# Performance work log

Measured on AMD Instinct MI355X. Metric: run time of the kernel, lower is better.

Reference implementation:

```python
import jax, jax.numpy as jnp
import numpy as np

N = 50000          # nodes
E = 1600000        # edges (avg degree 32)
H = 64             # hidden dim (module default x=64)
C = 10             # num_classes = max(y)+1
SLOPE = 0.01       # torch leaky_relu default


def _glorot(key, shape):
    lim = jnp.sqrt(6.0 / (shape[0] + shape[1]))
    return jax.random.uniform(key, shape, jnp.float32, -lim, lim)


def setup_inputs() -> dict:
    key = jax.random.key(0)
    ks = jax.random.split(key, 8)
    x = jax.random.normal(ks[0], (N, 1), jnp.float32)
    edge_index = jax.random.randint(ks[1], (2, E), 0, N, dtype=jnp.int64)
    W1 = _glorot(ks[2], (1, 10));  b1 = jnp.zeros((10,), jnp.float32)
    W2 = _glorot(ks[3], (10, H));  b2 = jnp.zeros((H,), jnp.float32)
    W3 = _glorot(ks[4], (H, H));   b3 = jnp.zeros((H,), jnp.float32)
    fcW = _glorot(ks[5], (H * N, C))
    fcb = jnp.zeros((C,), jnp.float32)
    return {"x": x, "edge_index": edge_index, "W1": W1, "b1": b1,
            "W2": W2, "b2": b2, "W3": W3, "b3": b3, "fcW": fcW, "fcb": fcb}


def _gcn_layer(h, W, b, src, dst, norm):
    # GCNConv: out = D^{-1/2} (A + I) D^{-1/2} (h W) + b
    h = h @ W                                   # [N, out]
    msg = h[src] * norm[:, None]                # gather + edge-scale
    agg = jax.ops.segment_sum(msg, dst, num_segments=N)  # scatter-add
    return agg + b


def reference(x, edge_index, W1, b1, W2, b2, W3, b3, fcW, fcb):
    src, dst = edge_index[0], edge_index[1]
    loop = jnp.arange(N, dtype=src.dtype)
    src_all = jnp.concatenate([src, loop])      # add self-loops
    dst_all = jnp.concatenate([dst, loop])
    deg = jax.ops.segment_sum(jnp.ones_like(dst_all, jnp.float32), dst_all,
                              num_segments=N)   # >= 1 due to self-loops
    dinv = jax.lax.rsqrt(deg)
    norm = dinv[src_all] * dinv[dst_all]        # per-edge normalization

    h = jax.nn.leaky_relu(_gcn_layer(x, W1, b1, src_all, dst_all, norm), SLOPE)
    h = jax.nn.leaky_relu(_gcn_layer(h, W2, b2, src_all, dst_all, norm), SLOPE)
    h = jax.nn.leaky_relu(_gcn_layer(h, W3, b3, src_all, dst_all, norm), SLOPE)

    logits = h.reshape(-1) @ fcW + fcb          # [C]
    return jax.nn.softmax(logits, axis=0)
```

## Files before the change

### kernel.cpp

```cpp
#include <hip/hip_runtime.h>
#include <hip/hip_fp16.h>
#include <hip/hip_fp8.h>


constexpr int F1  = 10;
constexpr int F1P = 16;
constexpr int HD  = 64;
constexpr int NC  = 10;
constexpr int LOGIT_BLOCKS = 2048;

constexpr int BSH   = 7;
constexpr int NBC   = 391;
constexpr int BCAPG = 5120;
constexpr int CSTR  = 16;
constexpr int LCAP  = 38;
constexpr int TILE  = 8192;

static __device__ __forceinline__ float lrelu(float v) {
    return v > 0.0f ? v : 0.01f * v;
}

#if defined(__has_builtin)
#if __has_builtin(__builtin_amdgcn_cvt_f32_fp8)
#define FP8_DECODE(w, c) __builtin_amdgcn_cvt_f32_fp8((int)(w), (c))
#endif
#endif
#ifndef FP8_DECODE
static __device__ __forceinline__ float fp8_decode_sw(unsigned w, int c) {
    __hip_fp8_e4m3 t; t.__x = (unsigned char)(w >> (8 * c)); return (float)t;
}
#define FP8_DECODE(w, c) fp8_decode_sw((w), (c))
#endif

static __device__ __forceinline__ unsigned char fp8_encode(float v) {
    __hip_fp8_e4m3 t(v);
    return (unsigned char)t.__x;
}

__global__ void k_bcur(int* __restrict__ bcur, int NB) {
    int b = blockIdx.x * blockDim.x + threadIdx.x;
    if (b < NB) bcur[b * CSTR] = b * BCAPG;
}

__global__ __launch_bounds__(512) void k_bucket(const int* __restrict__ src,
                                                const int* __restrict__ dst,
                                                int* __restrict__ bcur,
                                                unsigned* __restrict__ bpairs, int E) {
    __shared__ unsigned stage[NBC * LCAP];
    __shared__ int lcnt[NBC];
    for (int i = threadIdx.x; i < NBC; i += 512) lcnt[i] = 0;
    __syncthreads();
    int tile0 = blockIdx.x * TILE;
#pragma unroll
    for (int k = 0; k < TILE / 512; ++k) {
        int e = tile0 + k * 512 + threadIdx.x;
        if (e < E) {
            int d = dst[e];
            unsigned pk = (unsigned)src[e] | ((unsigned)(d & 127) << 16);
            int bb = d >> BSH;
            int pos = atomicAdd(&lcnt[bb], 1);
            if (pos < LCAP) stage[bb * LCAP + pos] = pk;
            else {
                int gp = atomicAdd(&bcur[bb * CSTR], 1);
                bpairs[gp] = pk;
            }
        }
    }
    __syncthreads();
    int wid = threadIdx.x >> 6, lane = threadIdx.x & 63;
    for (int bb = wid; bb < NBC; bb += 8) {
        int cntb = min(lcnt[bb], LCAP);
        if (cntb == 0) continue;
        int gp = 0;
        if (lane == 0) gp = atomicAdd(&bcur[bb * CSTR], cntb);
        gp = __shfl(gp, 0, 64);
        for (int i = lane; i < cntb; i += 64) bpairs[gp + i] = stage[bb * LCAP + i];
    }
}

__global__ __launch_bounds__(256) void k_fine(const int* __restrict__ bcur,
                                              const unsigned* __restrict__ bpairs,
                                              const float* __restrict__ x,
                                              unsigned short* __restrict__ csr,
                                              float* __restrict__ dinv,
                                              float* __restrict__ xs,
                                              int* __restrict__ rowbeg,
                                              int* __restrict__ rowend, int N) {
    __shared__ unsigned short lout[BCAPG];
    __shared__ int lcnt[128], lbeg[128];
    int b = blockIdx.x;
    int n0 = b << BSH;
    int nn = min(128, N - n0);
    int base = b * BCAPG;
    int nedges = bcur[b * CSTR] - base;
    for (int i = threadIdx.x; i < nn; i += 256) lcnt[i] = 0;
    __syncthreads();
    for (int i = threadIdx.x; i < nedges; i += 256)
        atomicAdd(&lcnt[(bpairs[base + i] >> 16) & 127], 1);
    __syncthreads();
    if (threadIdx.x == 0) {
        int acc = 0;
        for (int j = 0; j < nn; ++j) { lbeg[j] = acc; acc += lcnt[j]; }
    }
    __syncthreads();
    for (int i = threadIdx.x; i < nn; i += 256) {
        int node = n0 + i;
        float di = rsqrtf(1.0f + (float)lcnt[i]);
        dinv[node]   = di;
        xs[node]     = x[node] * di;
        rowbeg[node] = base + lbeg[i];
        rowend[node] = base + lbeg[i] + lcnt[i];
    }
    __syncthreads();
    for (int i = threadIdx.x; i < nn; i += 256) lcnt[i] = lbeg[i];
    __syncthreads();
    for (int i = threadIdx.x; i < nedges; i += 256) {
        unsigned p = bpairs[base + i];
        int pos = atomicAdd(&lcnt[(p >> 16) & 127], 1);
        lout[pos] = (unsigned short)(p & 0xFFFFu);
    }
    __syncthreads();
    for (int i = threadIdx.x; i < nedges; i += 256) csr[base + i] = lout[i];
}

__global__ void k_l1h1(const int* __restrict__ rowbeg, const int* __restrict__ rowend,
                       const unsigned short* __restrict__ csr,
                       const float* __restrict__ xs, const float* __restrict__ dinv,
                       const float* __restrict__ W1, const float* __restrict__ b1,
                       __half* __restrict__ h1s, int N) {
    int node = (blockIdx.x * blockDim.x + threadIdx.x) >> 6;
    int lane = threadIdx.x & 63;
    if (node >= N) return;
    int lo = rowbeg[node], hi = rowend[node];
    float acc = 0.0f;
    for (int j = lo + lane; j < hi; j += 64) acc += xs[csr[j]];
#pragma unroll
    for (int off = 32; off > 0; off >>= 1) acc += __shfl_xor(acc, off, 64);
    float di = dinv[node];
    float s = di * (acc + xs[node]);
    if (lane < F1P) {
        float h = (lane < F1) ? lrelu(s * W1[lane] + b1[lane]) * di : 0.0f;
        h1s[node * F1P + lane] = __float2half(h);
    }
}

__global__ __launch_bounds__(256, 4) void k_l2h2(const int* __restrict__ rowbeg,
                                                 const int* __restrict__ rowend,
                                                 const unsigned short* __restrict__ csr,
                                                 const __half* __restrict__ h1s,
                                                 const float* __restrict__ dinv,
                                                 const float* __restrict__ W2,
                                                 const float* __restrict__ b2,
                                                 unsigned char* __restrict__ h2s8, int N) {
    __shared__ float awork[4][12];
    int node = (blockIdx.x * blockDim.x + threadIdx.x) >> 6;
    int wid  = threadIdx.x >> 6;
    int lane = threadIdx.x & 63;
    bool valid = node < N;
    float w2r[F1];
#pragma unroll
    for (int k = 0; k < F1; ++k) w2r[k] = W2[k * HD + lane];
    int g = lane >> 3, f2 = lane & 7;
    int lo = 0, deg = 0;
    if (valid) { lo = rowbeg[node]; deg = rowend[node] - lo; }
    int myidx = (lane < deg) ? (int)csr[lo + lane] : 0;
    int nfull = min(deg, 64);
    float a0 = 0.0f, a1 = 0.0f;
#pragma unroll
    for (int j = 0; j < 64; j += 8) {
        if (j >= nfull) break;
        int e = j + g;
        int sn = __shfl(myidx, e, 64);
        if (e < nfull) {
            __half2 hv = *reinterpret_cast<const __half2*>(h1s + sn * F1P + f2 * 2);
            a0 += __low2float(hv);
            a1 += __high2float(hv);
        }
    }
    for (int j = 64; j < deg; j += 8) {
        int e = j + g;
        if (e < deg) {
            int sn = csr[lo + e];
            __half2 hv = *reinterpret_cast<const __half2*>(h1s + sn * F1P + f2 * 2);
            a0 += __low2float(hv);
            a1 += __high2float(hv);
        }
    }
    a0 += __shfl_xor(a0, 8, 64); a0 += __shfl_xor(a0, 16, 64); a0 += __shfl_xor(a0, 32, 64);
    a1 += __shfl_xor(a1, 8, 64); a1 += __shfl_xor(a1, 16, 64); a1 += __shfl_xor(a1, 32, 64);
    if (valid) {
        __half2 hs = *reinterpret_cast<const __half2*>(h1s + node * F1P + f2 * 2);
        a0 += __low2float(hs);
        a1 += __high2float(hs);
    }
    if (g == 0 && f2 < 5)
        *reinterpret_cast<float2*>(&awork[wid][f2 * 2]) = make_float2(a0, a1);
    __syncthreads();
    float4 av0 = *reinterpret_cast<const float4*>(&awork[wid][0]);
    float4 av1 = *reinterpret_cast<const float4*>(&awork[wid][4]);
    float2 av2 = *reinterpret_cast<const float2*>(&awork[wid][8]);
    float S = av0.x * w2r[0] + av0.y * w2r[1] + av0.z * w2r[2] + av0.w * w2r[3]
            + av1.x * w2r[4] + av1.y * w2r[5] + av1.z * w2r[6] + av1.w * w2r[7]
            + av2.x * w2r[8] + av2.y * w2r[9];
    if (valid) {
        float di = dinv[node];
        h2s8[node * HD + lane] = fp8_encode(lrelu(di * S + b2[lane]) * di);
    }
}

__global__ __launch_bounds__(256, 4) void k_l3h3(const int* __restrict__ rowbeg,
                                                 const int* __restrict__ rowend,
                                                 const unsigned short* __restrict__ csr,
                                                 const unsigned char* __restrict__ h2s8,
                                                 const float* __restrict__ dinv,
                                                 const float* __restrict__ W3,
                                                 const float* __restrict__ b3,
                                                 float* __restrict__ h3, int N) {
    __shared__ float awork[4][HD];
    int node = (blockIdx.x * blockDim.x + threadIdx.x) >> 6;
    int wid  = threadIdx.x >> 6;
    int lane = threadIdx.x & 63;
    bool valid = node < N;
    float w3r[HD];
#pragma unroll
    for (int k = 0; k < HD; ++k) w3r[k] = W3[k * HD + lane];
    int g = lane >> 4, q = lane & 15;
    int lo = 0, deg = 0;
    if (valid) { lo = rowbeg[node]; deg = rowend[node] - lo; }
    int myidx = (lane < deg) ? (int)csr[lo + lane] : 0;
    int nfull = min(deg, 64);
    float a0 = 0.0f, a1 = 0.0f, a2 = 0.0f, a3 = 0.0f;
#pragma unroll
    for (int j = 0; j < 64; j += 4) {
        if (j >= nfull) break;
        int e = j + g;
        int sn = __shfl(myidx, e, 64);
        if (e < nfull) {
            unsigned wv = *reinterpret_cast<const unsigned*>(h2s8 + sn * HD + q * 4);
            a0 += FP8_DECODE(wv, 0);
            a1 += FP8_DECODE(wv, 1);
            a2 += FP8_DECODE(wv, 2);
            a3 += FP8_DECODE(wv, 3);
        }
    }
    for (int j = 64; j < deg; j += 4) {
        int e = j + g;
        if (e < deg) {
            int sn = csr[lo + e];
            unsigned wv = *reinterpret_cast<const unsigned*>(h2s8 + sn * HD + q * 4);
            a0 += FP8_DECODE(wv, 0);
            a1 += FP8_DECODE(wv, 1);
            a2 += FP8_DECODE(wv, 2);
            a3 += FP8_DECODE(wv, 3);
        }
    }
    a0 += __shfl_xor(a0, 16, 64); a0 += __shfl_xor(a0, 32, 64);
    a1 += __shfl_xor(a1, 16, 64); a1 += __shfl_xor(a1, 32, 64);
    a2 += __shfl_xor(a2, 16, 64); a2 += __shfl_xor(a2, 32, 64);
    a3 += __shfl_xor(a3, 16, 64); a3 += __shfl_xor(a3, 32, 64);
    if (valid) {
        unsigned ws = *reinterpret_cast<const unsigned*>(h2s8 + node * HD + q * 4);
        a0 += FP8_DECODE(ws, 0);
        a1 += FP8_DECODE(ws, 1);
        a2 += FP8_DECODE(ws, 2);
        a3 += FP8_DECODE(ws, 3);
    }
    if (g == 0)
        *reinterpret_cast<float4*>(&awork[wid][q * 4]) = make_float4(a0, a1, a2, a3);
    __syncthreads();
    float S = 0.0f;
#pragma unroll
    for (int c = 0; c < 16; ++c) {
        float4 av = *reinterpret_cast<const float4*>(&awork[wid][c * 4]);
        S += av.x * w3r[4 * c]     + av.y * w3r[4 * c + 1]
           + av.z * w3r[4 * c + 2] + av.w * w3r[4 * c + 3];
    }
    if (valid) {
        float di = dinv[node];
        h3[node * HD + lane] = lrelu(di * S + b3[lane]);
    }
}

__global__ void k_logits_part(const float* __restrict__ h3,
                              const float4* __restrict__ fw4,
                              float* __restrict__ partial, int P ) {
    float acc[NC];
#pragma unroll
    for (int c = 0; c < NC; ++c) acc[c] = 0.0f;
    int nth = gridDim.x * blockDim.x;
    for (int p = blockIdx.x * blockDim.x + threadIdx.x; p < P; p += nth) {
        const float4* w = fw4 + (size_t)p * 5;
        float4 w0 = w[0], w1 = w[1], w2 = w[2], w3 = w[3], w4 = w[4];
        float2 hv = *reinterpret_cast<const float2*>(h3 + 2 * (size_t)p);
        acc[0] += hv.x * w0.x; acc[1] += hv.x * w0.y; acc[2] += hv.x * w0.z; acc[3] += hv.x * w0.w;
        acc[4] += hv.x * w1.x; acc[5] += hv.x * w1.y; acc[6] += hv.x * w1.z; acc[7] += hv.x * w1.w;
        acc[8] += hv.x * w2.x; acc[9] += hv.x * w2.y; acc[0] += hv.y * w2.z; acc[1] += hv.y * w2.w;
        acc[2] += hv.y * w3.x; acc[3] += hv.y * w3.y; acc[4] += hv.y * w3.z; acc[5] += hv.y * w3.w;
        acc[6] += hv.y * w4.x; acc[7] += hv.y * w4.y; acc[8] += hv.y * w4.z; acc[9] += hv.y * w4.w;
    }
#pragma unroll
    for (int c = 0; c < NC; ++c) {
        float v = acc[c];
#pragma unroll
        for (int off = 32; off > 0; off >>= 1) v += __shfl_down(v, off, 64);
        acc[c] = v;
    }
    __shared__ float ls[4][NC];
    int wid = threadIdx.x >> 6, lane = threadIdx.x & 63;
    if (lane == 0) {
#pragma unroll
        for (int c = 0; c < NC; ++c) ls[wid][c] = acc[c];
    }
    __syncthreads();
    if (threadIdx.x < NC) {
        float ssum = ls[0][threadIdx.x] + ls[1][threadIdx.x]
                   + ls[2][threadIdx.x] + ls[3][threadIdx.x];
        partial[blockIdx.x * NC + threadIdx.x] = ssum;
    }
}

__global__ __launch_bounds__(1024) void k_final(const float* __restrict__ partial, int nblk,
                                                const float* __restrict__ fcb,
                                                float* __restrict__ out) {
    __shared__ float ls[NC];
    if (threadIdx.x < NC) ls[threadIdx.x] = 0.0f;
    __syncthreads();
    const int NCHUNK = 1024 / NC;
    int c = threadIdx.x % NC;
    int chunk = threadIdx.x / NC;
    float ssum = 0.0f;
    if (chunk < NCHUNK)
        for (int i = chunk; i < nblk; i += NCHUNK) ssum += partial[i * NC + c];
    if (chunk < NCHUNK) atomicAdd(&ls[c], ssum);
    __syncthreads();
    if (threadIdx.x == 0) {
        float l[NC], m = -1e30f;
        for (int k = 0; k < NC; ++k) { l[k] = ls[k] + fcb[k]; m = fmaxf(m, l[k]); }
        float sum = 0.0f;
        for (int k = 0; k < NC; ++k) { l[k] = expf(l[k] - m); sum += l[k]; }
        float inv = 1.0f / sum;
        for (int k = 0; k < NC; ++k) out[k] = l[k] * inv;
    }
}

extern "C" void kernel_launch(void* const* d_in, const int* in_sizes, int n_in,
                              void* d_out, int out_size, void* d_ws, size_t ws_size,
                              hipStream_t stream) {
    const float* x   = (const float*)d_in[0];
    const int*   ei  = (const int*)d_in[1];
    const float* W1  = (const float*)d_in[2];
    const float* b1  = (const float*)d_in[3];
    const float* W2  = (const float*)d_in[4];
    const float* b2  = (const float*)d_in[5];
    const float* W3  = (const float*)d_in[6];
    const float* b3  = (const float*)d_in[7];
    const float* fcW = (const float*)d_in[8];
    const float* fcb = (const float*)d_in[9];
    float* out = (float*)d_out;

    const int N = in_sizes[0];
    const int E = in_sizes[1] / 2;
    const int* src = ei;
    const int* dst = ei + E;
    const int NB = (N + 127) >> BSH;

    char* w = (char*)d_ws;
    auto take = [&](size_t elems) { void* p = w; w += elems * 4; return p; };
    float* dinv    = (float*)take(N);
    int*   rowbeg  = (int*)  take(N);
    int*   rowend  = (int*)  take(N);
    int*   bcur    = (int*)  take((size_t)NB * CSTR);
    unsigned short* csr = (unsigned short*)take((size_t)NB * BCAPG / 2);
    float* xs      = (float*)take(N);
    __half* h1s    = (__half*)take((size_t)N * F1P / 2);
    unsigned char* h2s8 = (unsigned char*)take((size_t)N * HD / 4);
    float* h3      = (float*)take((size_t)N * HD);
    float* partial = xs;
    unsigned* bpairs = (unsigned*)h3;

    const int B = 256;
    auto cdiv = [](long long a, long long b) { return (int)((a + b - 1) / b); };

    k_bcur  <<<cdiv(NB, B), B, 0, stream>>>(bcur, NB);
    k_bucket<<<cdiv(E, TILE), 512, 0, stream>>>(src, dst, bcur, bpairs, E);
    k_fine  <<<NB, 256, 0, stream>>>(bcur, bpairs, x, csr, dinv, xs, rowbeg, rowend, N);

    k_l1h1<<<cdiv((long long)N * 64, B), B, 0, stream>>>(rowbeg, rowend, csr, xs, dinv, W1, b1, h1s, N);
    k_l2h2<<<cdiv((long long)N * 64, B), B, 0, stream>>>(rowbeg, rowend, csr, h1s, dinv, W2, b2, h2s8, N);
    k_l3h3<<<cdiv((long long)N * 64, B), B, 0, stream>>>(rowbeg, rowend, csr, h2s8, dinv, W3, b3, h3, N);

    const int P = (N * HD) / 2;
    k_logits_part<<<LOGIT_BLOCKS, B, 0, stream>>>(h3, (const float4*)fcW, partial, P);
    k_final<<<1, 1024, 0, stream>>>(partial, LOGIT_BLOCKS, fcb, out);
}
```

Before: 179.7 us.

## Split layer-3 matvec across waves and stage fcW via coalesced LDS loads

The layer-3 kernel now has each wave keep only 16 rows of W3 in registers and compute partial dot products for all four nodes in the block. The partials are reduced through a second shared buffer, which cuts register pressure and raises the launch-bounds occupancy target from 4 to 8 blocks. The logits kernel now loads fcW tiles into LDS with coalesced nontemporal loads before each thread reads its 5 float4s, and the number of logit blocks doubles. This aims to remove the strided 80-byte-per-thread global access to the large fcW matrix, at the cost of extra barriers and LDS traffic.

```diff
diff --git a/kernel.cpp b/kernel.cpp
--- a/kernel.cpp
+++ b/kernel.cpp
@@ -7,7 +7,7 @@
 constexpr int F1P = 16;
 constexpr int HD  = 64;
 constexpr int NC  = 10;
-constexpr int LOGIT_BLOCKS = 2048;
+constexpr int LOGIT_BLOCKS = 4096;
 
 constexpr int BSH   = 7;
 constexpr int NBC   = 391;
@@ -15,6 +15,8 @@
 constexpr int CSTR  = 16;
 constexpr int LCAP  = 38;
 constexpr int TILE  = 8192;
+
+using f32x4 = __attribute__((ext_vector_type(4))) float;
 
 static __device__ __forceinline__ float lrelu(float v) {
     return v > 0.0f ? v : 0.01f * v;
@@ -208,7 +210,7 @@
     }
 }
 
-__global__ __launch_bounds__(256, 4) void k_l3h3(const int* __restrict__ rowbeg,
+__global__ __launch_bounds__(256, 8) void k_l3h3(const int* __restrict__ rowbeg,
                                                  const int* __restrict__ rowend,
                                                  const unsigned short* __restrict__ csr,
                                                  const unsigned char* __restrict__ h2s8,
@@ -217,13 +219,14 @@
                                                  const float* __restrict__ b3,
                                                  float* __restrict__ h3, int N) {
     __shared__ float awork[4][HD];
+    __shared__ float plds[64][20];
     int node = (blockIdx.x * blockDim.x + threadIdx.x) >> 6;
     int wid  = threadIdx.x >> 6;
     int lane = threadIdx.x & 63;
     bool valid = node < N;
-    float w3r[HD];
-#pragma unroll
-    for (int k = 0; k < HD; ++k) w3r[k] = W3[k * HD + lane];
+    float w3r[16];
+#pragma unroll
+    for (int j = 0; j < 16; ++j) w3r[j] = W3[(16 * wid + j) * HD + lane];
     int g = lane >> 4, q = lane & 15;
     int lo = 0, deg = 0;
     if (valid) { lo = rowbeg[node]; deg = rowend[node] - lo; }
@@ -268,35 +271,51 @@
     if (g == 0)
         *reinterpret_cast<float4*>(&awork[wid][q * 4]) = make_float4(a0, a1, a2, a3);
     __syncthreads();
-    float S = 0.0f;
-#pragma unroll
-    for (int c = 0; c < 16; ++c) {
-        float4 av = *reinterpret_cast<const float4*>(&awork[wid][c * 4]);
-        S += av.x * w3r[4 * c]     + av.y * w3r[4 * c + 1]
-           + av.z * w3r[4 * c + 2] + av.w * w3r[4 * c + 3];
-    }
+#pragma unroll
+    for (int n = 0; n < 4; ++n) {
+        float p = 0.0f;
+#pragma unroll
+        for (int jj = 0; jj < 4; ++jj) {
+            float4 av = *reinterpret_cast<const float4*>(&awork[n][16 * wid + 4 * jj]);
+            p += av.x * w3r[4 * jj]     + av.y * w3r[4 * jj + 1]
+               + av.z * w3r[4 * jj + 2] + av.w * w3r[4 * jj + 3];
+        }
+        plds[lane][n * 4 + wid] = p;
+    }
+    __syncthreads();
     if (valid) {
+        float4 pv = *reinterpret_cast<const float4*>(&plds[lane][wid * 4]);
+        float S = (pv.x + pv.y) + (pv.z + pv.w);
         float di = dinv[node];
         h3[node * HD + lane] = lrelu(di * S + b3[lane]);
     }
 }
 
-__global__ void k_logits_part(const float* __restrict__ h3,
-                              const float4* __restrict__ fw4,
-                              float* __restrict__ partial, int P ) {
+__global__ __launch_bounds__(256) void k_logits_part(const float* __restrict__ h3,
+                                                     const f32x4* __restrict__ fw4,
+                                                     float* __restrict__ partial,
+                                                     int P ) {
+    __shared__ f32x4 stage[1280];
     float acc[NC];
 #pragma unroll
     for (int c = 0; c < NC; ++c) acc[c] = 0.0f;
-    int nth = gridDim.x * blockDim.x;
-    for (int p = blockIdx.x * blockDim.x + threadIdx.x; p < P; p += nth) {
-        const float4* w = fw4 + (size_t)p * 5;
-        float4 w0 = w[0], w1 = w[1], w2 = w[2], w3 = w[3], w4 = w[4];
-        float2 hv = *reinterpret_cast<const float2*>(h3 + 2 * (size_t)p);
-        acc[0] += hv.x * w0.x; acc[1] += hv.x * w0.y; acc[2] += hv.x * w0.z; acc[3] += hv.x * w0.w;
-        acc[4] += hv.x * w1.x; acc[5] += hv.x * w1.y; acc[6] += hv.x * w1.z; acc[7] += hv.x * w1.w;
-        acc[8] += hv.x * w2.x; acc[9] += hv.x * w2.y; acc[0] += hv.y * w2.z; acc[1] += hv.y * w2.w;
-        acc[2] += hv.y * w3.x; acc[3] += hv.y * w3.y; acc[4] += hv.y * w3.z; acc[5] += hv.y * w3.w;
-        acc[6] += hv.y * w4.x; acc[7] += hv.y * w4.y; acc[8] += hv.y * w4.z; acc[9] += hv.y * w4.w;
+    for (int pbase = blockIdx.x * 256; pbase < P; pbase += gridDim.x * 256) {
+        int nfl = min(256, P - pbase) * 5;
+        __syncthreads();
+        for (int i = threadIdx.x; i < nfl; i += 256)
+            stage[i] = __builtin_nontemporal_load(&fw4[(size_t)pbase * 5 + i]);
+        __syncthreads();
+        int p = pbase + threadIdx.x;
+        if (p < P) {
+            const f32x4* w = &stage[threadIdx.x * 5];
+            f32x4 w0 = w[0], w1 = w[1], w2 = w[2], w3 = w[3], w4 = w[4];
+            float2 hv = *reinterpret_cast<const float2*>(h3 + 2 * (size_t)p);
+            acc[0] += hv.x * w0.x; acc[1] += hv.x * w0.y; acc[2] += hv.x * w0.z; acc[3] += hv.x * w0.w;
+            acc[4] += hv.x * w1.x; acc[5] += hv.x * w1.y; acc[6] += hv.x * w1.z; acc[7] += hv.x * w1.w;
+            acc[8] += hv.x * w2.x; acc[9] += hv.x * w2.y; acc[0] += hv.y * w2.z; acc[1] += hv.y * w2.w;
+            acc[2] += hv.y * w3.x; acc[3] += hv.y * w3.y; acc[4] += hv.y * w3.z; acc[5] += hv.y * w3.w;
+            acc[6] += hv.y * w4.x; acc[7] += hv.y * w4.y; acc[8] += hv.y * w4.z; acc[9] += hv.y * w4.w;
+        }
     }
 #pragma unroll
     for (int c = 0; c < NC; ++c) {
@@ -390,6 +409,6 @@
     k_l3h3<<<cdiv((long long)N * 64, B), B, 0, stream>>>(rowbeg, rowend, csr, h2s8, dinv, W3, b3, h3, N);
 
     const int P = (N * HD) / 2;
-    k_logits_part<<<LOGIT_BLOCKS, B, 0, stream>>>(h3, (const float4*)fcW, partial, P);
+    k_logits_part<<<LOGIT_BLOCKS, B, 0, stream>>>(h3, (const f32x4*)fcW, partial, P);
     k_final<<<1, 1024, 0, stream>>>(partial, LOGIT_BLOCKS, fcb, out);
 }
```

New measurement: 171.2 us (median of 2 runs). -4.7%, faster.
